# Kernel optimization log

Measured on AMD Instinct MI355X. Metric: run time of the kernel, lower is better.

## Reference

```python
import math
import jax, jax.numpy as jnp
import numpy as np

H = 16  # head_count
D = 1024  # model_dim
DH = D // H  # dim_per_head = 64
PAD_IDX = 1


def setup_inputs() -> dict:
    key = jax.random.key(0)
    ks = jax.random.split(key, 16)
    B, L = 4, 512
    s = 0.02
    inp = {
        'key': jax.random.normal(ks[0], (B, L, D), jnp.float32),
        'value': jax.random.normal(ks[1], (B, L, D), jnp.float32),
        'query': jax.random.normal(ks[2], (B, L, D), jnp.float32),
        'ast_parents_matrix': jax.random.randint(ks[3], (B, L, L), 0, 200, jnp.int32),
        'mask': jnp.zeros((B, 1, L), jnp.bool_),
        'Wq': jax.random.normal(ks[4], (D, D), jnp.float32) * s,
        'bq': jnp.zeros((D,), jnp.float32),
        'Wk': jax.random.normal(ks[5], (D, D), jnp.float32) * s,
        'bk': jnp.zeros((D,), jnp.float32),
        'Wv': jax.random.normal(ks[6], (D, D), jnp.float32) * s,
        'bv': jnp.zeros((D,), jnp.float32),
        'Wo': jax.random.normal(ks[7], (D, D), jnp.float32) * s,
        'bo': jnp.zeros((D,), jnp.float32),
        'struct_emb': jax.random.normal(ks[8], (200, DH), jnp.float32).at[PAD_IDX].set(0.0),
        'value_emb': jax.random.normal(ks[9], (10000, DH), jnp.float32).at[PAD_IDX].set(0.0),
    }
    return inp


def _parent_embeddings(matrix, struct_emb, value_emb):
    # matrix: (B, Lq, K) int ids; even key positions use structure vocab, odd use value vocab
    B, Lq, K = matrix.shape
    s_ids = matrix[:, :, ::2]   # (B, Lq, ceil(K/2))
    v_ids = matrix[:, :, 1::2]  # (B, Lq, floor(K/2))
    emb_s = struct_emb[s_ids]   # (B, Lq, S, DH)
    emb_v = value_emb[v_ids]    # (B, Lq, V, DH)
    S = emb_s.shape[2]
    if emb_v.shape[2] != S:  # odd K: pad value stream by one zero slot, drop after interleave
        emb_v = jnp.concatenate([emb_v, jnp.zeros_like(emb_s[:, :, :1])], axis=2)
    pe = jnp.stack([emb_s, emb_v], axis=3).reshape(B, Lq, 2 * S, DH)
    return pe[:, :, :K, :]  # (B, Lq, K, DH)


def reference(key, value, query, ast_parents_matrix, mask,
              Wq, bq, Wk, bk, Wv, bv, Wo, bo, struct_emb, value_emb):
    B, L, _ = query.shape

    def shape(x):
        return x.reshape(B, -1, H, DH).transpose(0, 2, 1, 3)  # (B,H,L,DH)

    q = shape(query @ Wq + bq) / math.sqrt(DH)
    k = shape(key @ Wk + bk)
    v = shape(value @ Wv + bv)

    qk = jnp.einsum('bhid,bhjd->bhij', q, k)  # (B,H,L,L)

    pe = _parent_embeddings(ast_parents_matrix[:, :, :L], struct_emb, value_emb)
    score_ast = jnp.einsum('bhid,bijd->bhij', q, pe)

    scores = (qk + score_ast).astype(jnp.float32)
    scores = jnp.where(mask[:, None, :, :], -1e18, scores)  # mask: (B,1,L)->(B,1,1,L)
    attn = jax.nn.softmax(scores, axis=-1).astype(q.dtype)
    # dropout p=0.0 (eval) -> identity
    context = jnp.einsum('bhij,bhjd->bhid', attn, v)  # (B,H,L,DH)
    context = context.transpose(0, 2, 1, 3).reshape(B, L, D)
    output = context @ Wo + bo
    return output, attn
```

## Files before the change

### kernel.cpp

```cpp
#include <hip/hip_runtime.h>
#include <cstddef>

#define H 16
#define D 1024
#define DH 64
#define L 512

typedef __attribute__((ext_vector_type(8))) short bf16x8;
typedef __attribute__((ext_vector_type(4))) short bf16x4;
typedef __attribute__((ext_vector_type(4))) float f32x4;

__device__ inline short f2bf(float x) {
    union { float f; unsigned u; } c; c.f = x;
    unsigned r = (c.u + 0x7FFFu + ((c.u >> 16) & 1u)) >> 16;
    return (short)r;
}
__device__ inline float bf2f(short x) {
    union { float f; unsigned u; } c;
    c.u = ((unsigned)(unsigned short)x) << 16; return c.f;
}

__device__ inline void gload_lds16(const void* g, void* l) {
    __builtin_amdgcn_global_load_lds(
        (const __attribute__((address_space(1))) unsigned int*)g,
        (__attribute__((address_space(3))) unsigned int*)l,
        16, 0, 0);
}

struct PrepArgs {
    const float* csrc[5]; short* cdst[5]; int cn[5];
    const float* W[4]; short* T[4];
};

__global__ __launch_bounds__(256) void prep_kernel(PrepArgs a) {
    const int y = blockIdx.y;
    if (y < 5) {
        const float* s = a.csrc[y];
        short* d = a.cdst[y];
        int n = a.cn[y];
        int i = (blockIdx.x * 256 + threadIdx.x) * 8;
        if (i >= n) return;
        float4 x0 = *(const float4*)(s + i);
        float4 x1 = *(const float4*)(s + i + 4);
        bf16x8 o;
        o[0] = f2bf(x0.x); o[1] = f2bf(x0.y); o[2] = f2bf(x0.z); o[3] = f2bf(x0.w);
        o[4] = f2bf(x1.x); o[5] = f2bf(x1.y); o[6] = f2bf(x1.z); o[7] = f2bf(x1.w);
        *(bf16x8*)(d + i) = o;
    } else {
        const float* W = a.W[y - 5];
        short* T = a.T[y - 5];
        int idx = blockIdx.x * 256 + threadIdx.x;
        if (idx >= 1024 * 128) return;
        int n = idx & 1023;
        int k0 = (idx >> 10) << 3;
        bf16x8 o;
        #pragma unroll
        for (int kk = 0; kk < 8; ++kk)
            o[kk] = f2bf(W[(size_t)(k0 + kk) * 1024 + n]);
        *(bf16x8*)(T + (size_t)n * 1024 + k0) = o;
    }
}

#define BM 128
#define BN 64
#define BKK 64

struct GemmBatch {
    const short* A[3]; const short* Bt[3]; const float* bias[3];
    void* out[3]; float scale[3]; int mode[3];
};

__global__ __launch_bounds__(256) void gemm_mfma_kernel(GemmBatch P, int M, int N, int K) {
    const int z = blockIdx.z;
    const short* __restrict__ A  = P.A[z];
    const short* __restrict__ Bt = P.Bt[z];
    const float* __restrict__ bias = P.bias[z];
    const float scale = P.scale[z];
    const int mode = P.mode[z];

    __shared__ short lds[(BM + BN) * BKK];
    short* As = lds;
    short* Bs = lds + BM * BKK;

    const int tid = threadIdx.x;
    const int wave = tid >> 6, lane = tid & 63;
    const int fm = lane & 15, quad = lane >> 4;
    const int m0 = blockIdx.y * BM, n0 = blockIdx.x * BN;

    int arow[4], acol[4];
    #pragma unroll
    for (int t = 0; t < 4; ++t) {
        int s = (wave * 4 + t) * 64 + lane;
        int row = s >> 3;
        int u = (s & 7) ^ (row & 7);
        arow[t] = row; acol[t] = u * 8;
    }
    int brow[2], bcol[2];
    #pragma unroll
    for (int t = 0; t < 2; ++t) {
        int s = (wave * 2 + t) * 64 + lane;
        int row = s >> 3;
        int u = (s & 7) ^ (row & 7);
        brow[t] = row; bcol[t] = u * 8;
    }

    int aoff[2][2], boff[4][2];
    #pragma unroll
    for (int mt = 0; mt < 2; ++mt)
        #pragma unroll
        for (int kst = 0; kst < 2; ++kst) {
            int row = wave * 32 + mt * 16 + fm;
            int u = quad + 4 * kst;
            aoff[mt][kst] = row * 64 + ((u ^ (row & 7)) * 8);
        }
    #pragma unroll
    for (int nt = 0; nt < 4; ++nt)
        #pragma unroll
        for (int kst = 0; kst < 2; ++kst) {
            int row = nt * 16 + fm;
            int u = quad + 4 * kst;
            boff[nt][kst] = row * 64 + ((u ^ (row & 7)) * 8);
        }

    f32x4 acc[2][4];
    #pragma unroll
    for (int mt = 0; mt < 2; ++mt)
        #pragma unroll
        for (int nt = 0; nt < 4; ++nt) acc[mt][nt] = (f32x4){0.f, 0.f, 0.f, 0.f};

    for (int k0 = 0; k0 < K; k0 += BKK) {
        __syncthreads();
        #pragma unroll
        for (int t = 0; t < 4; ++t)
            gload_lds16(A + (size_t)(m0 + arow[t]) * K + k0 + acol[t],
                        As + (wave * 4 + t) * 512);
        #pragma unroll
        for (int t = 0; t < 2; ++t)
            gload_lds16(Bt + (size_t)(n0 + brow[t]) * K + k0 + bcol[t],
                        Bs + (wave * 2 + t) * 512);
        __syncthreads();
        #pragma unroll
        for (int kst = 0; kst < 2; ++kst) {
            bf16x8 af[2], bfr[4];
            af[0] = *(const bf16x8*)(As + aoff[0][kst]);
            af[1] = *(const bf16x8*)(As + aoff[1][kst]);
            #pragma unroll
            for (int nt = 0; nt < 4; ++nt)
                bfr[nt] = *(const bf16x8*)(Bs + boff[nt][kst]);
            #pragma unroll
            for (int mt = 0; mt < 2; ++mt)
                #pragma unroll
                for (int nt = 0; nt < 4; ++nt)
                    acc[mt][nt] = __builtin_amdgcn_mfma_f32_16x16x32_bf16(
                        af[mt], bfr[nt], acc[mt][nt], 0, 0, 0);
        }
    }

    if (mode == 2) {
        __syncthreads();
        short (*T)[BM + 8] = (short(*)[BM + 8])&lds[0];
        #pragma unroll
        for (int mt = 0; mt < 2; ++mt)
            #pragma unroll
            for (int nt = 0; nt < 4; ++nt) {
                int nn = nt * 16 + fm;
                float bv = bias[n0 + nn];
                #pragma unroll
                for (int r = 0; r < 4; ++r) {
                    int mm = wave * 32 + mt * 16 + quad * 4 + r;
                    T[nn][mm] = f2bf((acc[mt][nt][r] + bv) * scale);
                }
            }
        __syncthreads();
        int b = m0 >> 9;
        int ibase = m0 & (L - 1);
        int hblk = n0 >> 6;
        int n = tid >> 2, seg = (tid & 3) * 32;
        short* dst = (short*)P.out[z] + (((size_t)(b * H + hblk) * DH + n) * L) + ibase + seg;
        #pragma unroll
        for (int c = 0; c < 4; ++c)
            *(bf16x8*)(dst + c * 8) = *(const bf16x8*)(&T[n][seg + c * 8]);
    } else {
        #pragma unroll
        for (int mt = 0; mt < 2; ++mt)
            #pragma unroll
            for (int nt = 0; nt < 4; ++nt) {
                int n = n0 + nt * 16 + fm;
                float bv = bias[n];
                #pragma unroll
                for (int r = 0; r < 4; ++r) {
                    int m = m0 + wave * 32 + mt * 16 + quad * 4 + r;
                    float val = (acc[mt][nt][r] + bv) * scale;
                    if (mode == 0) {
                        ((float*)P.out[z])[(size_t)m * N + n] = val;
                    } else {
                        int b = m >> 9, i = m & (L - 1);
                        int h = n >> 6, d = n & (DH - 1);
                        ((short*)P.out[z])[(((size_t)(b * H + h) * L + i) * DH) + d] = f2bf(val);
                    }
                }
            }
    }
}

__global__ __launch_bounds__(256) void ast_kernel(
    const short* __restrict__ Qb, const int* __restrict__ mat,
    const short* __restrict__ semb, const short* __restrict__ vemb,
    short* __restrict__ Sast)
{
    const int i = blockIdx.x, b = blockIdx.y;
    const int tid = threadIdx.x;
    const int wave = tid >> 6, lane = tid & 63;
    const int fm = lane & 15, quad = lane >> 4;
    __shared__ short Sl[H][L + 8];

    const short* qp = Qb + (((size_t)(b * H + fm) * L + i) * DH);
    bf16x8 a0 = *(const bf16x8*)(qp + quad * 8);
    bf16x8 a1 = *(const bf16x8*)(qp + 32 + quad * 8);

    const int* mrow = mat + ((size_t)b * L + i) * L;

    int idxs[8];
    const short* ebase[8];
    #pragma unroll
    for (int t = 0; t < 8; ++t) {
        int j = (wave + t * 4) * 16 + fm;
        idxs[t] = mrow[j];
    }
    #pragma unroll
    for (int t = 0; t < 8; ++t) {
        int j = (wave + t * 4) * 16 + fm;
        ebase[t] = ((j & 1) ? vemb : semb) + (size_t)idxs[t] * DH;
    }

    #pragma unroll
    for (int t = 0; t < 8; ++t) {
        int j = (wave + t * 4) * 16 + fm;
        bf16x8 b0 = *(const bf16x8*)(ebase[t] + quad * 8);
        bf16x8 b1 = *(const bf16x8*)(ebase[t] + 32 + quad * 8);
        f32x4 c = {0.f, 0.f, 0.f, 0.f};
        c = __builtin_amdgcn_mfma_f32_16x16x32_bf16(a0, b0, c, 0, 0, 0);
        c = __builtin_amdgcn_mfma_f32_16x16x32_bf16(a1, b1, c, 0, 0, 0);
        #pragma unroll
        for (int r = 0; r < 4; ++r)
            Sl[quad * 4 + r][j] = f2bf(c[r]);
    }
    __syncthreads();
    int hh = tid >> 4, j0 = (tid & 15) * 32;
    short* dst = Sast + ((((size_t)b * L + i) * H + hh) * L) + j0;
    #pragma unroll
    for (int c = 0; c < 4; ++c)
        *(bf16x8*)(dst + c * 8) = *(const bf16x8*)(&Sl[hh][j0 + c * 8]);
}

#define PPITCH 520

__global__ __launch_bounds__(256, 2) void attn_fused_kernel(
    const short* __restrict__ Qb, const short* __restrict__ Kb,
    const short* __restrict__ Vt, const short* __restrict__ Sast,
    const unsigned char* __restrict__ mask,
    float* __restrict__ attn, short* __restrict__ ctx)
{
    const int i0 = blockIdx.x * 64;
    const int h = blockIdx.y;
    const int b = blockIdx.z;
    const int tid = threadIdx.x;
    const int wave = tid >> 6, lane = tid & 63;
    const int fm = lane & 15, quad = lane >> 4;

    __shared__ short Pb[64 * PPITCH];

    {
        const short* base = Sast + (((size_t)b * L + i0) * H + h) * L;
        #pragma unroll
        for (int p = 0; p < 16; ++p) {
            int row = p * 4 + (tid >> 6);
            int col = (tid & 63) * 8;
            *(bf16x8*)(&Pb[row * PPITCH + col]) =
                *(const bf16x8*)(base + (size_t)row * (H * L) + col);
        }
    }

    const int iw = i0 + wave * 16;
    const short* qp = Qb + (((size_t)(b * H + h) * L + iw + fm) * DH);
    bf16x8 q0 = *(const bf16x8*)(qp + quad * 8);
    bf16x8 q1 = *(const bf16x8*)(qp + 32 + quad * 8);
    const short* Kbase = Kb + ((size_t)(b * H + h) * L) * DH;
    const unsigned char* mrow = mask + (size_t)b * L;

    __syncthreads();

    short* Prow = &Pb[(wave * 16 + fm) * PPITCH];

    float s[32][4];
    float mx = -3.0e38f;
    #pragma unroll
    for (int t = 0; t < 32; ++t) {
        const short* kr = Kbase + (size_t)(t * 16 + fm) * DH;
        bf16x8 k0 = *(const bf16x8*)(kr + quad * 8);
        bf16x8 k1 = *(const bf16x8*)(kr + 32 + quad * 8);
        f32x4 c = {0.f, 0.f, 0.f, 0.f};
        c = __builtin_amdgcn_mfma_f32_16x16x32_bf16(k0, q0, c, 0, 0, 0);
        c = __builtin_amdgcn_mfma_f32_16x16x32_bf16(k1, q1, c, 0, 0, 0);
        bf16x4 sa = *(const bf16x4*)(&Prow[t * 16 + quad * 4]);
        unsigned mku = *(const unsigned*)(mrow + t * 16 + quad * 4);
        #pragma unroll
        for (int r = 0; r < 4; ++r) {
            float sv = c[r] + bf2f(sa[r]);
            sv = ((mku >> (8 * r)) & 255u) ? -1e18f : sv;
            s[t][r] = sv;
            mx = fmaxf(mx, sv);
        }
    }

    mx = fmaxf(mx, __shfl_xor(mx, 16));
    mx = fmaxf(mx, __shfl_xor(mx, 32));

    float sum = 0.f;
    #pragma unroll
    for (int t = 0; t < 32; ++t)
        #pragma unroll
        for (int r = 0; r < 4; ++r) {
            float e = __expf(s[t][r] - mx);
            s[t][r] = e;
            sum += e;
        }
    sum += __shfl_xor(sum, 16);
    sum += __shfl_xor(sum, 32);
    float inv = 1.f / sum;

    float* arow = attn + (((size_t)(b * H + h) * L + iw + fm) * L);
    #pragma unroll
    for (int t = 0; t < 32; ++t) {
        bf16x4 pw;
        #pragma unroll
        for (int r = 0; r < 4; ++r)
            pw[r] = f2bf(s[t][r] * inv);
        *(bf16x4*)(&Prow[t * 16 + quad * 4]) = pw;
        float4 v;
        v.x = bf2f(pw[0]); v.y = bf2f(pw[1]); v.z = bf2f(pw[2]); v.w = bf2f(pw[3]);
        *(float4*)(arow + t * 16 + quad * 4) = v;
    }

    const short* Vbase = Vt + ((size_t)(b * H + h) * DH) * L;
    f32x4 o[4];
    #pragma unroll
    for (int dt = 0; dt < 4; ++dt) o[dt] = (f32x4){0.f, 0.f, 0.f, 0.f};
    #pragma unroll
    for (int ks = 0; ks < L; ks += 32) {
        bf16x8 pa = *(const bf16x8*)(&Prow[ks + quad * 8]);
        #pragma unroll
        for (int dt = 0; dt < 4; ++dt) {
            bf16x8 vb = *(const bf16x8*)(Vbase + (size_t)(dt * 16 + fm) * L + ks + quad * 8);
            o[dt] = __builtin_amdgcn_mfma_f32_16x16x32_bf16(pa, vb, o[dt], 0, 0, 0);
        }
    }
    #pragma unroll
    for (int dt = 0; dt < 4; ++dt)
        #pragma unroll
        for (int r = 0; r < 4; ++r)
            ctx[((size_t)b * L + iw + quad * 4 + r) * D + h * DH + dt * 16 + fm] = f2bf(o[dt][r]);
}

extern "C" void kernel_launch(void* const* d_in, const int* in_sizes, int n_in,
                              void* d_out, int out_size, void* d_ws, size_t ws_size,
                              hipStream_t stream) {
    const float* key_in   = (const float*)d_in[0];
    const float* value_in = (const float*)d_in[1];
    const float* query_in = (const float*)d_in[2];
    const int*   mat      = (const int*)d_in[3];
    const unsigned char* mask = (const unsigned char*)d_in[4];
    const float* Wq = (const float*)d_in[5];
    const float* bq = (const float*)d_in[6];
    const float* Wk = (const float*)d_in[7];
    const float* bk = (const float*)d_in[8];
    const float* Wv = (const float*)d_in[9];
    const float* bv = (const float*)d_in[10];
    const float* Wo = (const float*)d_in[11];
    const float* bo = (const float*)d_in[12];
    const float* struct_emb = (const float*)d_in[13];
    const float* value_emb  = (const float*)d_in[14];

    const int B = in_sizes[2] / (L * D);
    const int M = B * L;

    short* p = (short*)d_ws;
    short* xk  = p;  p += (size_t)M * D;
    short* xv  = p;  p += (size_t)M * D;
    short* xq  = p;  p += (size_t)M * D;
    short* WqT = p;  p += (size_t)D * D;
    short* WkT = p;  p += (size_t)D * D;
    short* WvT = p;  p += (size_t)D * D;
    short* WoT = p;  p += (size_t)D * D;
    short* semb = p; p += 16384;
    short* vemb = p; p += (size_t)in_sizes[14];
    short* Qb = p;   p += (size_t)M * D;
    short* Kb = p;   p += (size_t)M * D;
    short* Vt = p;   p += (size_t)M * D;
    short* Sast = p; p += (size_t)B * L * H * L;
    short* ctx = xk;

    float* out_p  = (float*)d_out;
    float* attn_p = out_p + (size_t)M * D;

    PrepArgs pa;
    pa.csrc[0] = key_in;     pa.cdst[0] = xk;   pa.cn[0] = M * D;
    pa.csrc[1] = value_in;   pa.cdst[1] = xv;   pa.cn[1] = M * D;
    pa.csrc[2] = query_in;   pa.cdst[2] = xq;   pa.cn[2] = M * D;
    pa.csrc[3] = struct_emb; pa.cdst[3] = semb; pa.cn[3] = in_sizes[13];
    pa.csrc[4] = value_emb;  pa.cdst[4] = vemb; pa.cn[4] = in_sizes[14];
    pa.W[0] = Wq; pa.W[1] = Wk; pa.W[2] = Wv; pa.W[3] = Wo;
    pa.T[0] = WqT; pa.T[1] = WkT; pa.T[2] = WvT; pa.T[3] = WoT;
    prep_kernel<<<dim3((M * D) / 2048, 9), 256, 0, stream>>>(pa);

    GemmBatch qkv;
    qkv.A[0] = xq; qkv.Bt[0] = WqT; qkv.bias[0] = bq; qkv.out[0] = Qb; qkv.scale[0] = 0.125f; qkv.mode[0] = 1;
    qkv.A[1] = xk; qkv.Bt[1] = WkT; qkv.bias[1] = bk; qkv.out[1] = Kb; qkv.scale[1] = 1.0f;   qkv.mode[1] = 1;
    qkv.A[2] = xv; qkv.Bt[2] = WvT; qkv.bias[2] = bv; qkv.out[2] = Vt; qkv.scale[2] = 1.0f;   qkv.mode[2] = 2;
    gemm_mfma_kernel<<<dim3(D / BN, M / BM, 3), 256, 0, stream>>>(qkv, M, D, D);

    ast_kernel<<<dim3(L, B), 256, 0, stream>>>(Qb, mat, semb, vemb, Sast);

    attn_fused_kernel<<<dim3(L / 64, H, B), 256, 0, stream>>>(
        Qb, Kb, Vt, Sast, mask, attn_p, ctx);

    GemmBatch fin;
    fin.A[0] = ctx; fin.Bt[0] = WoT; fin.bias[0] = bo; fin.out[0] = out_p; fin.scale[0] = 1.0f; fin.mode[0] = 0;
    fin.A[1] = ctx; fin.Bt[1] = WoT; fin.bias[1] = bo; fin.out[1] = out_p; fin.scale[1] = 1.0f; fin.mode[1] = 0;
    fin.A[2] = ctx; fin.Bt[2] = WoT; fin.bias[2] = bo; fin.out[2] = out_p; fin.scale[2] = 1.0f; fin.mode[2] = 0;
    gemm_mfma_kernel<<<dim3(D / BN, M / BM, 1), 256, 0, stream>>>(fin, M, D, D);
}
```

Before: 237.4 us.

## Split attention key dimension across waves with cross-wave softmax reduction

```diff
diff --git a/kernel.cpp b/kernel.cpp
--- a/kernel.cpp
+++ b/kernel.cpp
@@ -253,56 +253,43 @@
         *(bf16x8*)(dst + c * 8) = *(const bf16x8*)(&Sl[hh][j0 + c * 8]);
 }
 
-#define PPITCH 520
-
-__global__ __launch_bounds__(256, 2) void attn_fused_kernel(
+__global__ __launch_bounds__(256, 4) void attn_fused_kernel(
     const short* __restrict__ Qb, const short* __restrict__ Kb,
     const short* __restrict__ Vt, const short* __restrict__ Sast,
     const unsigned char* __restrict__ mask,
     float* __restrict__ attn, short* __restrict__ ctx)
 {
-    const int i0 = blockIdx.x * 64;
+    const int i0 = blockIdx.x * 16;
     const int h = blockIdx.y;
     const int b = blockIdx.z;
     const int tid = threadIdx.x;
     const int wave = tid >> 6, lane = tid & 63;
     const int fm = lane & 15, quad = lane >> 4;
-
-    __shared__ short Pb[64 * PPITCH];
-
-    {
-        const short* base = Sast + (((size_t)b * L + i0) * H + h) * L;
-        #pragma unroll
-        for (int p = 0; p < 16; ++p) {
-            int row = p * 4 + (tid >> 6);
-            int col = (tid & 63) * 8;
-            *(bf16x8*)(&Pb[row * PPITCH + col]) =
-                *(const bf16x8*)(base + (size_t)row * (H * L) + col);
-        }
-    }
-
-    const int iw = i0 + wave * 16;
-    const short* qp = Qb + (((size_t)(b * H + h) * L + iw + fm) * DH);
+    const int jw = wave * 128;
+
+    __shared__ short Pl[16][520];
+    __shared__ float red_m[4][16];
+    __shared__ float red_l[4][16];
+
+    const short* qp = Qb + (((size_t)(b * H + h) * L + i0 + fm) * DH);
     bf16x8 q0 = *(const bf16x8*)(qp + quad * 8);
     bf16x8 q1 = *(const bf16x8*)(qp + 32 + quad * 8);
     const short* Kbase = Kb + ((size_t)(b * H + h) * L) * DH;
-    const unsigned char* mrow = mask + (size_t)b * L;
-
-    __syncthreads();
-
-    short* Prow = &Pb[(wave * 16 + fm) * PPITCH];
-
-    float s[32][4];
+    const short* sastrow = Sast + (((size_t)b * L + i0 + fm) * H + h) * L;
+    const unsigned char* mrow = mask + (size_t)b * L + jw;
+
+    float s[8][4];
     float mx = -3.0e38f;
     #pragma unroll
-    for (int t = 0; t < 32; ++t) {
-        const short* kr = Kbase + (size_t)(t * 16 + fm) * DH;
+    for (int t = 0; t < 8; ++t) {
+        int jt = jw + t * 16;
+        const short* kr = Kbase + (size_t)(jt + fm) * DH;
         bf16x8 k0 = *(const bf16x8*)(kr + quad * 8);
         bf16x8 k1 = *(const bf16x8*)(kr + 32 + quad * 8);
         f32x4 c = {0.f, 0.f, 0.f, 0.f};
         c = __builtin_amdgcn_mfma_f32_16x16x32_bf16(k0, q0, c, 0, 0, 0);
         c = __builtin_amdgcn_mfma_f32_16x16x32_bf16(k1, q1, c, 0, 0, 0);
-        bf16x4 sa = *(const bf16x4*)(&Prow[t * 16 + quad * 4]);
+        bf16x4 sa = *(const bf16x4*)(sastrow + jt + quad * 4);
         unsigned mku = *(const unsigned*)(mrow + t * 16 + quad * 4);
         #pragma unroll
         for (int r = 0; r < 4; ++r) {
@@ -318,7 +305,7 @@
 
     float sum = 0.f;
     #pragma unroll
-    for (int t = 0; t < 32; ++t)
+    for (int t = 0; t < 8; ++t)
         #pragma unroll
         for (int r = 0; r < 4; ++r) {
             float e = __expf(s[t][r] - mx);
@@ -327,39 +314,47 @@
         }
     sum += __shfl_xor(sum, 16);
     sum += __shfl_xor(sum, 32);
-    float inv = 1.f / sum;
-
-    float* arow = attn + (((size_t)(b * H + h) * L + iw + fm) * L);
-    #pragma unroll
-    for (int t = 0; t < 32; ++t) {
+    if (quad == 0) {
+        red_m[wave][fm] = mx;
+        red_l[wave][fm] = sum;
+    }
+    __syncthreads();
+
+    float m0_ = red_m[0][fm], m1_ = red_m[1][fm];
+    float m2_ = red_m[2][fm], m3_ = red_m[3][fm];
+    float M_ = fmaxf(fmaxf(m0_, m1_), fmaxf(m2_, m3_));
+    float T_ = red_l[0][fm] * __expf(m0_ - M_)
+             + red_l[1][fm] * __expf(m1_ - M_)
+             + red_l[2][fm] * __expf(m2_ - M_)
+             + red_l[3][fm] * __expf(m3_ - M_);
+    float fac = __expf(mx - M_) / T_;
+
+    float* arow = attn + (((size_t)(b * H + h) * L + i0 + fm) * L);
+    #pragma unroll
+    for (int t = 0; t < 8; ++t) {
+        int jt = jw + t * 16 + quad * 4;
         bf16x4 pw;
         #pragma unroll
         for (int r = 0; r < 4; ++r)
-            pw[r] = f2bf(s[t][r] * inv);
-        *(bf16x4*)(&Prow[t * 16 + quad * 4]) = pw;
+            pw[r] = f2bf(s[t][r] * fac);
+        *(bf16x4*)(&Pl[fm][jt]) = pw;
         float4 v;
         v.x = bf2f(pw[0]); v.y = bf2f(pw[1]); v.z = bf2f(pw[2]); v.w = bf2f(pw[3]);
-        *(float4*)(arow + t * 16 + quad * 4) = v;
-    }
-
-    const short* Vbase = Vt + ((size_t)(b * H + h) * DH) * L;
-    f32x4 o[4];
-    #pragma unroll
-    for (int dt = 0; dt < 4; ++dt) o[dt] = (f32x4){0.f, 0.f, 0.f, 0.f};
+        *(float4*)(arow + jt) = v;
+    }
+    __syncthreads();
+
+    const short* Vb = Vt + (((size_t)(b * H + h) * DH + wave * 16 + fm) * L);
+    f32x4 o = {0.f, 0.f, 0.f, 0.f};
     #pragma unroll
     for (int ks = 0; ks < L; ks += 32) {
-        bf16x8 pa = *(const bf16x8*)(&Prow[ks + quad * 8]);
-        #pragma unroll
-        for (int dt = 0; dt < 4; ++dt) {
-            bf16x8 vb = *(const bf16x8*)(Vbase + (size_t)(dt * 16 + fm) * L + ks + quad * 8);
-            o[dt] = __builtin_amdgcn_mfma_f32_16x16x32_bf16(pa, vb, o[dt], 0, 0, 0);
-        }
-    }
-    #pragma unroll
-    for (int dt = 0; dt < 4; ++dt)
-        #pragma unroll
-        for (int r = 0; r < 4; ++r)
-            ctx[((size_t)b * L + iw + quad * 4 + r) * D + h * DH + dt * 16 + fm] = f2bf(o[dt][r]);
+        bf16x8 pa = *(const bf16x8*)(&Pl[fm][ks + quad * 8]);
+        bf16x8 vb = *(const bf16x8*)(Vb + ks + quad * 8);
+        o = __builtin_amdgcn_mfma_f32_16x16x32_bf16(pa, vb, o, 0, 0, 0);
+    }
+    #pragma unroll
+    for (int r = 0; r < 4; ++r)
+        ctx[((size_t)b * L + i0 + quad * 4 + r) * D + h * DH + wave * 16 + fm] = f2bf(o[r]);
 }
 
 extern "C" void kernel_launch(void* const* d_in, const int* in_sizes, int n_in,
@@ -421,7 +416,7 @@
 
     ast_kernel<<<dim3(L, B), 256, 0, stream>>>(Qb, mat, semb, vemb, Sast);
 
-    attn_fused_kernel<<<dim3(L / 64, H, B), 256, 0, stream>>>(
+    attn_fused_kernel<<<dim3(L / 16, H, B), 256, 0, stream>>>(
         Qb, Kb, Vt, Sast, mask, attn_p, ctx);
 
     GemmBatch fin;
```

Result: no change. 240.8 us (+1.4%).
